# Performance work log

Measured on AMD Instinct MI355X. Metric: run time of the kernel, lower is better.

The kernel has to match this reference:

```python
import jax, jax.numpy as jnp
import numpy as np

D = 2048
N_HEADS = 16
N_KV = 4
HEAD_DIM = D // N_HEADS  # 128
N_REP = N_HEADS // N_KV  # 4
B, S = 2, 2048


def setup_inputs() -> dict:
    key = jax.random.key(0)
    ks = jax.random.split(key, 5)
    scale = 0.02
    return {
        "x": jax.random.normal(ks[0], (B, S, D), dtype=jnp.float32),
        "wq": jax.random.normal(ks[1], (D, N_HEADS * HEAD_DIM), dtype=jnp.float32) * scale,
        "wk": jax.random.normal(ks[2], (D, N_KV * HEAD_DIM), dtype=jnp.float32) * scale,
        "wv": jax.random.normal(ks[3], (D, N_KV * HEAD_DIM), dtype=jnp.float32) * scale,
        "wo": jax.random.normal(ks[4], (N_HEADS * HEAD_DIM, D), dtype=jnp.float32) * scale,
    }


def reference(x, wq, wk, wv, wo):
    b, s, _ = x.shape
    # projections
    xq = (x @ wq).reshape(b, s, N_HEADS, HEAD_DIM)
    xk = (x @ wk).reshape(b, s, N_KV, HEAD_DIM)
    xv = (x @ wv).reshape(b, s, N_KV, HEAD_DIM)
    # GQA: group queries per kv head -> [b, n_kv, n_rep, s, d]
    xq = xq.transpose(0, 2, 1, 3).reshape(b, N_KV, N_REP, s, HEAD_DIM)
    xk = xk.transpose(0, 2, 1, 3)  # [b, n_kv, s, d]
    xv = xv.transpose(0, 2, 1, 3)
    scale = 1.0 / jnp.sqrt(jnp.asarray(HEAD_DIM, dtype=x.dtype))
    scores = jnp.einsum('bkrqd,bkvd->bkrqv', xq, xk) * scale  # [b,n_kv,n_rep,s,s]
    causal = jnp.triu(jnp.ones((s, s), dtype=bool), k=1)
    scores = jnp.where(causal, jnp.asarray(-jnp.inf, dtype=scores.dtype), scores)
    probs = jax.nn.softmax(scores, axis=-1)
    out = jnp.einsum('bkrqv,bkvd->bkrqd', probs, xv)  # [b,n_kv,n_rep,s,d]
    out = out.reshape(b, N_HEADS, s, HEAD_DIM).transpose(0, 2, 1, 3).reshape(b, s, N_HEADS * HEAD_DIM)
    return out @ wo
```

## Files before the change

kernel.cpp:

```cpp
#include <hip/hip_runtime.h>

typedef unsigned short u16;
using bf16x8 = __attribute__((ext_vector_type(8))) short;
using bf16x4 = __attribute__((ext_vector_type(4))) short;
using f32x4  = __attribute__((ext_vector_type(4))) float;

#define ATTN_NEG (-3.0e38f)

#if __has_builtin(__builtin_amdgcn_mfma_f32_16x16x16_bf16)
__device__ __forceinline__ f32x4 mfma16(bf16x4 a, bf16x4 b, f32x4 c) {
  return __builtin_amdgcn_mfma_f32_16x16x16_bf16(a, b, c, 0, 0, 0);
}
#elif __has_builtin(__builtin_amdgcn_mfma_f32_16x16x16bf16_1k)
__device__ __forceinline__ f32x4 mfma16(bf16x4 a, bf16x4 b, f32x4 c) {
  return __builtin_amdgcn_mfma_f32_16x16x16bf16_1k(a, b, c, 0, 0, 0);
}
#else
__device__ __forceinline__ f32x4 mfma16(bf16x4 a, bf16x4 b, f32x4 c) {
  asm volatile("v_mfma_f32_16x16x16_bf16 %0, %1, %2, %3"
               : "=v"(c) : "v"(a), "v"(b), "v"(c));
  return c;
}
#endif

__device__ __forceinline__ u16 f2bf_rne(float f) {
  unsigned int u = __float_as_uint(f);
  u += 0x7fffu + ((u >> 16) & 1u);
  return (u16)(u >> 16);
}

__device__ __forceinline__ void load_lds16(const u16* g, u16* l) {
  using gp = const __attribute__((address_space(1))) unsigned int*;
  using lp = __attribute__((address_space(3))) unsigned int*;
  __builtin_amdgcn_global_load_lds((gp)g, (lp)l, 16, 0, 0);
}

__device__ __forceinline__ void transpose_body(const float* __restrict__ in,
                                               u16* __restrict__ out, int K, int N,
                                               int bx, int by, int tid) {
  __shared__ float tile[32][33];
  int tx = tid & 31, ty = tid >> 5;
  int x0 = bx * 32, y0 = by * 32;
  #pragma unroll
  for (int i = 0; i < 32; i += 8)
    tile[ty + i][tx] = in[(size_t)(y0 + ty + i) * N + x0 + tx];
  __syncthreads();
  #pragma unroll
  for (int i = 0; i < 32; i += 8)
    out[(size_t)(x0 + ty + i) * K + y0 + tx] = f2bf_rne(tile[tx][ty + i]);
}

__global__ __launch_bounds__(256) void prep_kernel(const float* __restrict__ x,
                                                   const float* __restrict__ wq,
                                                   const float* __restrict__ wk,
                                                   const float* __restrict__ wv,
                                                   const float* __restrict__ wo,
                                                   u16* xb, u16* wqt, u16* wkt, u16* wvt,
                                                   u16* wot) {
  int bid = blockIdx.x, tid = threadIdx.x;
  if (bid < 8192) {
    int i = bid * 1024 + tid * 4;
    float4 v = *(const float4*)(x + i);
    u16* p = xb + i;
    p[0] = f2bf_rne(v.x); p[1] = f2bf_rne(v.y); p[2] = f2bf_rne(v.z); p[3] = f2bf_rne(v.w);
  } else if (bid < 12288) {
    int t = bid - 8192;
    transpose_body(wq, wqt, 2048, 2048, t & 63, t >> 6, tid);
  } else if (bid < 13312) {
    int t = bid - 12288;
    transpose_body(wk, wkt, 2048, 512, t & 15, t >> 4, tid);
  } else if (bid < 14336) {
    int t = bid - 13312;
    transpose_body(wv, wvt, 2048, 512, t & 15, t >> 4, tid);
  } else {
    int t = bid - 14336;
    transpose_body(wo, wot, 2048, 2048, t & 63, t >> 6, tid);
  }
}

template <int MODE>
__device__ __forceinline__ void gemm_tile(const u16* __restrict__ A, const u16* __restrict__ Bt,
                                          void* __restrict__ Cv, int M, int N, int K,
                                          int bx, int by, char* smem) {
  u16* As = (u16*)smem;
  u16* Bs = (u16*)(smem + 8192);
  const int tid  = threadIdx.x;
  const int wave = tid >> 6, lane = tid & 63;
  const int quad = lane >> 4, l16 = lane & 15;
  const int m0 = by * 128, n0 = bx * 128;
  const int wm = (wave >> 1) * 64, wn = (wave & 1) * 64;
  f32x4 acc[4][4] = {};

  const int srow = (wave << 4) + (lane >> 2);
  const int scol = (lane & 3) << 3;
  const u16* ga0 = A  + (size_t)(m0 + srow) * K + scol;
  const u16* gb0 = Bt + (size_t)(n0 + srow) * K + scol;
  u16* la = As + wave * 512;
  u16* lb = Bs + wave * 512;

  for (int k0 = 0; k0 < K; k0 += 32) {
    __syncthreads();
    load_lds16(ga0 + k0, la);
    load_lds16(ga0 + (size_t)64 * K + k0, la + 2048);
    load_lds16(gb0 + k0, lb);
    load_lds16(gb0 + (size_t)64 * K + k0, lb + 2048);
    __syncthreads();
    bf16x8 af[4], bfr[4];
    #pragma unroll
    for (int i = 0; i < 4; ++i) {
      af[i]  = *(const bf16x8*)(As + (wm + i * 16 + l16) * 32 + quad * 8);
      bfr[i] = *(const bf16x8*)(Bs + (wn + i * 16 + l16) * 32 + quad * 8);
    }
    #pragma unroll
    for (int mi = 0; mi < 4; ++mi)
      #pragma unroll
      for (int ni = 0; ni < 4; ++ni)
        acc[mi][ni] = __builtin_amdgcn_mfma_f32_16x16x32_bf16(af[mi], bfr[ni], acc[mi][ni], 0, 0, 0);
  }

  if constexpr (MODE == 0 || MODE == 3) {
    const float sc = (MODE == 3) ? 0.12751742f : 1.0f;
    u16* Cb = (u16*)Cv;
    #pragma unroll
    for (int mi = 0; mi < 4; ++mi)
      #pragma unroll
      for (int ni = 0; ni < 4; ++ni) {
        int row = m0 + wm + mi * 16 + quad * 4;
        int col = n0 + wn + ni * 16 + l16;
        #pragma unroll
        for (int r = 0; r < 4; ++r)
          Cb[(size_t)(row + r) * N + col] = f2bf_rne(acc[mi][ni][r] * sc);
      }
  } else if constexpr (MODE == 1) {
    u16* Cb = (u16*)Cv;
    #pragma unroll
    for (int mi = 0; mi < 4; ++mi)
      #pragma unroll
      for (int ni = 0; ni < 4; ++ni) {
        int col = n0 + wn + ni * 16 + l16;
        #pragma unroll
        for (int r = 0; r < 4; ++r) {
          int row = m0 + wm + mi * 16 + quad * 4 + r;
          int bb = row >> 11, s = row & 2047;
          int c = s & 31;
          int cp = ((c & 15) >> 2) * 8 + ((c >> 4) & 1) * 4 + (c & 3);
          Cb[((size_t)(bb * 512 + col)) * 2048 + (s & ~31) + cp] = f2bf_rne(acc[mi][ni][r]);
        }
      }
  } else {
    float* Cf = (float*)Cv;
    #pragma unroll
    for (int mi = 0; mi < 4; ++mi)
      #pragma unroll
      for (int ni = 0; ni < 4; ++ni) {
        int row = m0 + wm + mi * 16 + quad * 4;
        int col = n0 + wn + ni * 16 + l16;
        #pragma unroll
        for (int r = 0; r < 4; ++r)
          Cf[(size_t)(row + r) * N + col] = acc[mi][ni][r];
      }
  }
}

__global__ __launch_bounds__(256) void qkv_gemm(const u16* xb, const u16* wqt, const u16* wkt,
                                                const u16* wvt, u16* Qb, u16* Kb, u16* Vt) {
  extern __shared__ char smem[];
  int bx = blockIdx.x, by = blockIdx.y;
  if (bx < 16)
    gemm_tile<3>(xb, wqt, Qb, 4096, 2048, 2048, bx, by, smem);
  else if (bx < 20)
    gemm_tile<0>(xb, wkt, Kb, 4096, 512, 2048, bx - 16, by, smem);
  else
    gemm_tile<1>(xb, wvt, Vt, 4096, 512, 2048, bx - 20, by, smem);
}

template <int MODE>
__global__ __launch_bounds__(256) void gemm_kernel(const u16* A, const u16* Bt, void* C,
                                                   int M, int N, int K) {
  extern __shared__ char smem[];
  gemm_tile<MODE>(A, Bt, C, M, N, K, blockIdx.x, blockIdx.y, smem);
}


__device__ __forceinline__ void stage_kv(const u16* __restrict__ Kg, const u16* __restrict__ Vg,
                                         int kt0, u16* __restrict__ kbuf, u16* __restrict__ vbuf,
                                         int wave, int quad, int l16) {
  #pragma unroll
  for (int h = 0; h < 2; ++h)
    load_lds16(Kg + (size_t)(kt0 + h * 16 + l16) * 512 + wave * 32 + quad * 8,
               kbuf + (wave * 2 + h) * 512);
  #pragma unroll
  for (int i = 0; i < 2; ++i) {
    int f = wave * 2 + i;
    load_lds16(Vg + (size_t)(16 * f + l16) * 2048 + kt0 + quad * 8, vbuf + f * 512);
  }
}

template <bool MASKED>
__device__ __forceinline__ void attn_compute(const u16* __restrict__ kbuf,
                                             const u16* __restrict__ vbuf,
                                             int kt0, int q0w, int quad, int l16,
                                             const bf16x8 (&qf)[4], f32x4 (&o)[8],
                                             float& l_lane) {
  const int slot = (quad * 16 + l16) * 8;
  bf16x8 kf[8];
  #pragma unroll
  for (int kk = 0; kk < 8; ++kk) kf[kk] = *(const bf16x8*)(kbuf + kk * 512 + slot);

  f32x4 sa[2] = {};
  #pragma unroll
  for (int h = 0; h < 2; ++h)
    #pragma unroll
    for (int ks = 0; ks < 4; ++ks)
      sa[h] = __builtin_amdgcn_mfma_f32_16x16x32_bf16(kf[ks * 2 + h], qf[ks], sa[h], 0, 0, 0);

  bf16x4 pa[2];
  #pragma unroll
  for (int h = 0; h < 2; ++h) {
    #pragma unroll
    for (int r = 0; r < 4; ++r) {
      float s = sa[h][r];
      if (MASKED) {
        int kpos = kt0 + 16 * h + quad * 4 + r;
        s = (kpos <= q0w + l16) ? s : ATTN_NEG;
      }
      float p = __builtin_amdgcn_exp2f(s);
      l_lane += p;
      pa[h][r] = (short)f2bf_rne(p);
    }
  }

  #pragma unroll
  for (int f = 0; f < 8; ++f) {
    bf16x8 v8 = *(const bf16x8*)(vbuf + f * 512 + slot);
    bf16x4 vlo = {v8[0], v8[1], v8[2], v8[3]};
    bf16x4 vhi = {v8[4], v8[5], v8[6], v8[7]};
    o[f] = mfma16(pa[0], vlo, o[f]);
    o[f] = mfma16(pa[1], vhi, o[f]);
  }
}

__global__ __launch_bounds__(256, 2) void attn_kernel(const u16* __restrict__ Qb,
                                                      const u16* __restrict__ Kb,
                                                      const u16* __restrict__ Vt,
                                                      u16* __restrict__ Ob) {
  constexpr int S = 2048;
  const int b = blockIdx.z, h = blockIdx.y, g = h >> 2, tp = blockIdx.x;
  const int tid = threadIdx.x;
  const int wave = tid >> 6, lane = tid & 63, quad = lane >> 4, l16 = lane & 15;
  __shared__ alignas(16) u16 Kt[2][4096];
  __shared__ alignas(16) u16 Vl[2][4096];
  __shared__ float lbuf[4][16];

  const u16* Kg = Kb + (size_t)b * S * 512 + g * 128;
  const u16* Vg = Vt + (size_t)(b * 512 + g * 128) * 2048;

  #pragma unroll
  for (int half = 0; half < 2; ++half) {
    const int tile = (half == 0) ? tp : 31 - tp;
    const int wrow = (half == 0) ? wave : 3 - wave;
    const int q0w = tile * 64 + wrow * 16;
    const int nsteps = 2 * tile + 2;
    const int s_diag = 2 * tile + (wrow >> 1);

    bf16x8 qf[4];
    const u16* qrow = Qb + (size_t)(b * S + q0w + l16) * 2048 + h * 128 + quad * 8;
    #pragma unroll
    for (int ks = 0; ks < 4; ++ks) qf[ks] = *(const bf16x8*)(qrow + ks * 32);

    f32x4 o[8] = {};
    float l_lane = 0.f;

    __syncthreads();
    stage_kv(Kg, Vg, 0, Kt[0], Vl[0], wave, quad, l16);

    for (int s = 0; s < nsteps; ++s) {
      __syncthreads();
      if (s + 1 < nsteps)
        stage_kv(Kg, Vg, (s + 1) * 32, Kt[(s + 1) & 1], Vl[(s + 1) & 1], wave, quad, l16);
      if (s < s_diag)
        attn_compute<false>(Kt[s & 1], Vl[s & 1], s * 32, q0w, quad, l16, qf, o, l_lane);
      else if (s == s_diag)
        attn_compute<true>(Kt[s & 1], Vl[s & 1], s * 32, q0w, quad, l16, qf, o, l_lane);
    }

    float lt = l_lane + __shfl_xor(l_lane, 16);
    lt += __shfl_xor(lt, 32);
    if (quad == 0) lbuf[wave][l16] = lt;
    __builtin_amdgcn_wave_barrier();
    float il[4];
    #pragma unroll
    for (int r = 0; r < 4; ++r) il[r] = 1.f / lbuf[wave][quad * 4 + r];

    u16* orow = Ob + (size_t)(b * S + q0w + quad * 4) * 2048 + h * 128 + l16;
    #pragma unroll
    for (int f = 0; f < 8; ++f)
      #pragma unroll
      for (int r = 0; r < 4; ++r)
        orow[(size_t)r * 2048 + f * 16] = f2bf_rne(o[f][r] * il[r]);
  }
}

extern "C" void kernel_launch(void* const* d_in, const int* in_sizes, int n_in,
                              void* d_out, int out_size, void* d_ws, size_t ws_size,
                              hipStream_t stream) {
  const float* x  = (const float*)d_in[0];
  const float* wq = (const float*)d_in[1];
  const float* wk = (const float*)d_in[2];
  const float* wv = (const float*)d_in[3];
  const float* wo = (const float*)d_in[4];
  float* out = (float*)d_out;
  char* ws = (char*)d_ws;

  u16* xb  = (u16*)(ws);
  u16* wqt = (u16*)(ws + 16777216);
  u16* wkt = (u16*)(ws + 25165824);
  u16* wvt = (u16*)(ws + 27262976);
  u16* wot = (u16*)(ws + 29360128);
  u16* Qb  = (u16*)(ws + 37748736);
  u16* Kb  = (u16*)(ws + 54525952);
  u16* Vt  = (u16*)(ws + 58720256);
  u16* Ab  = (u16*)(ws + 62914560);

  prep_kernel<<<18432, 256, 0, stream>>>(x, wq, wk, wv, wo, xb, wqt, wkt, wvt, wot);
  qkv_gemm<<<dim3(24, 32), 256, 16384, stream>>>(xb, wqt, wkt, wvt, Qb, Kb, Vt);
  attn_kernel<<<dim3(16, 16, 2), 256, 0, stream>>>(Qb, Kb, Vt, Ab);
  gemm_kernel<2><<<dim3(16, 32), 256, 16384, stream>>>(Ab, wot, out, 4096, 2048, 2048);
}
```

Baseline: 311.8 us.

## Split KV steps across wave pairs with 32-row query tiles and LDS merge

Result: slower. 331.9 us (+6.5%).

```diff
diff --git a/kernel.cpp b/kernel.cpp
--- a/kernel.cpp
+++ b/kernel.cpp
@@ -197,46 +197,54 @@
 }
 
 template <bool MASKED>
-__device__ __forceinline__ void attn_compute(const u16* __restrict__ kbuf,
-                                             const u16* __restrict__ vbuf,
-                                             int kt0, int q0w, int quad, int l16,
-                                             const bf16x8 (&qf)[4], f32x4 (&o)[8],
-                                             float& l_lane) {
+__device__ __forceinline__ void attn_compute2(const u16* __restrict__ kbuf,
+                                              const u16* __restrict__ vbuf,
+                                              int kt0, int q0p, int quad, int l16,
+                                              const bf16x8 (&qf)[2][4], f32x4 (&o)[2][8],
+                                              float (&l_lane)[2]) {
   const int slot = (quad * 16 + l16) * 8;
   bf16x8 kf[8];
   #pragma unroll
   for (int kk = 0; kk < 8; ++kk) kf[kk] = *(const bf16x8*)(kbuf + kk * 512 + slot);
 
-  f32x4 sa[2] = {};
-  #pragma unroll
-  for (int h = 0; h < 2; ++h)
-    #pragma unroll
-    for (int ks = 0; ks < 4; ++ks)
-      sa[h] = __builtin_amdgcn_mfma_f32_16x16x32_bf16(kf[ks * 2 + h], qf[ks], sa[h], 0, 0, 0);
-
-  bf16x4 pa[2];
-  #pragma unroll
-  for (int h = 0; h < 2; ++h) {
-    #pragma unroll
-    for (int r = 0; r < 4; ++r) {
-      float s = sa[h][r];
-      if (MASKED) {
-        int kpos = kt0 + 16 * h + quad * 4 + r;
-        s = (kpos <= q0w + l16) ? s : ATTN_NEG;
-      }
-      float p = __builtin_amdgcn_exp2f(s);
-      l_lane += p;
-      pa[h][r] = (short)f2bf_rne(p);
-    }
-  }
+  f32x4 sa[2][2] = {};
+  #pragma unroll
+  for (int j = 0; j < 2; ++j)
+    #pragma unroll
+    for (int h = 0; h < 2; ++h)
+      #pragma unroll
+      for (int ks = 0; ks < 4; ++ks)
+        sa[j][h] = __builtin_amdgcn_mfma_f32_16x16x32_bf16(kf[ks * 2 + h], qf[j][ks],
+                                                           sa[j][h], 0, 0, 0);
+
+  bf16x4 pa[2][2];
+  #pragma unroll
+  for (int j = 0; j < 2; ++j)
+    #pragma unroll
+    for (int h = 0; h < 2; ++h) {
+      #pragma unroll
+      for (int r = 0; r < 4; ++r) {
+        float s = sa[j][h][r];
+        if (MASKED) {
+          int kpos = kt0 + 16 * h + quad * 4 + r;
+          s = (kpos <= q0p + j * 16 + l16) ? s : ATTN_NEG;
+        }
+        float p = __builtin_amdgcn_exp2f(s);
+        l_lane[j] += p;
+        pa[j][h][r] = (short)f2bf_rne(p);
+      }
+    }
 
   #pragma unroll
   for (int f = 0; f < 8; ++f) {
     bf16x8 v8 = *(const bf16x8*)(vbuf + f * 512 + slot);
     bf16x4 vlo = {v8[0], v8[1], v8[2], v8[3]};
     bf16x4 vhi = {v8[4], v8[5], v8[6], v8[7]};
-    o[f] = mfma16(pa[0], vlo, o[f]);
-    o[f] = mfma16(pa[1], vhi, o[f]);
+    #pragma unroll
+    for (int j = 0; j < 2; ++j) {
+      o[j][f] = mfma16(pa[j][0], vlo, o[j][f]);
+      o[j][f] = mfma16(pa[j][1], vhi, o[j][f]);
+    }
   }
 }
 
@@ -248,56 +256,94 @@
   const int b = blockIdx.z, h = blockIdx.y, g = h >> 2, tp = blockIdx.x;
   const int tid = threadIdx.x;
   const int wave = tid >> 6, lane = tid & 63, quad = lane >> 4, l16 = lane & 15;
-  __shared__ alignas(16) u16 Kt[2][4096];
-  __shared__ alignas(16) u16 Vl[2][4096];
-  __shared__ float lbuf[4][16];
+  const int pair = wave >> 1, wpar = wave & 1;
+  __shared__ alignas(16) u16 sraw[16384];
+  __shared__ float lmrg[2][128];
+  __shared__ float lbuf[2][2][16];
+
+  u16* Ktb = sraw;
+  u16* Vlb = sraw + 8192;
 
   const u16* Kg = Kb + (size_t)b * S * 512 + g * 128;
   const u16* Vg = Vt + (size_t)(b * 512 + g * 128) * 2048;
 
-  #pragma unroll
   for (int half = 0; half < 2; ++half) {
     const int tile = (half == 0) ? tp : 31 - tp;
-    const int wrow = (half == 0) ? wave : 3 - wave;
-    const int q0w = tile * 64 + wrow * 16;
+    const int q0p = tile * 64 + pair * 32;
     const int nsteps = 2 * tile + 2;
-    const int s_diag = 2 * tile + (wrow >> 1);
-
-    bf16x8 qf[4];
-    const u16* qrow = Qb + (size_t)(b * S + q0w + l16) * 2048 + h * 128 + quad * 8;
-    #pragma unroll
-    for (int ks = 0; ks < 4; ++ks) qf[ks] = *(const bf16x8*)(qrow + ks * 32);
-
-    f32x4 o[8] = {};
-    float l_lane = 0.f;
-
-    __syncthreads();
-    stage_kv(Kg, Vg, 0, Kt[0], Vl[0], wave, quad, l16);
+    const int s_diag = 2 * tile + pair;
+    const int par = wpar ^ half;
+
+    bf16x8 qf[2][4];
+    #pragma unroll
+    for (int j = 0; j < 2; ++j) {
+      const u16* qrow = Qb + (size_t)(b * S + q0p + j * 16 + l16) * 2048 + h * 128 + quad * 8;
+      #pragma unroll
+      for (int ks = 0; ks < 4; ++ks) qf[j][ks] = *(const bf16x8*)(qrow + ks * 32);
+    }
+
+    f32x4 o[2][8] = {};
+    float l_lane[2] = {0.f, 0.f};
+
+    __syncthreads();
+    stage_kv(Kg, Vg, 0, Ktb, Vlb, wave, quad, l16);
 
     for (int s = 0; s < nsteps; ++s) {
       __syncthreads();
+      const u16* kb = Ktb + (s & 1) * 4096;
+      const u16* vb = Vlb + (s & 1) * 4096;
       if (s + 1 < nsteps)
-        stage_kv(Kg, Vg, (s + 1) * 32, Kt[(s + 1) & 1], Vl[(s + 1) & 1], wave, quad, l16);
-      if (s < s_diag)
-        attn_compute<false>(Kt[s & 1], Vl[s & 1], s * 32, q0w, quad, l16, qf, o, l_lane);
-      else if (s == s_diag)
-        attn_compute<true>(Kt[s & 1], Vl[s & 1], s * 32, q0w, quad, l16, qf, o, l_lane);
-    }
-
-    float lt = l_lane + __shfl_xor(l_lane, 16);
-    lt += __shfl_xor(lt, 32);
-    if (quad == 0) lbuf[wave][l16] = lt;
-    __builtin_amdgcn_wave_barrier();
-    float il[4];
-    #pragma unroll
-    for (int r = 0; r < 4; ++r) il[r] = 1.f / lbuf[wave][quad * 4 + r];
-
-    u16* orow = Ob + (size_t)(b * S + q0w + quad * 4) * 2048 + h * 128 + l16;
-    #pragma unroll
-    for (int f = 0; f < 8; ++f)
-      #pragma unroll
-      for (int r = 0; r < 4; ++r)
-        orow[(size_t)r * 2048 + f * 16] = f2bf_rne(o[f][r] * il[r]);
+        stage_kv(Kg, Vg, (s + 1) * 32, Ktb + ((s + 1) & 1) * 4096,
+                 Vlb + ((s + 1) & 1) * 4096, wave, quad, l16);
+      if (((s & 1) == par) && s <= s_diag) {
+        if (s == s_diag)
+          attn_compute2<true>(kb, vb, s * 32, q0p, quad, l16, qf, o, l_lane);
+        else
+          attn_compute2<false>(kb, vb, s * 32, q0p, quad, l16, qf, o, l_lane);
+      }
+    }
+
+    __syncthreads();
+    if (wpar) {
+      float* mb = (float*)sraw + pair * 4096 + lane * 64;
+      #pragma unroll
+      for (int j = 0; j < 2; ++j)
+        #pragma unroll
+        for (int f = 0; f < 8; ++f)
+          *(f32x4*)(mb + j * 32 + f * 4) = o[j][f];
+      lmrg[pair][lane] = l_lane[0];
+      lmrg[pair][64 + lane] = l_lane[1];
+    }
+    __syncthreads();
+    if (!wpar) {
+      const float* mb = (const float*)sraw + pair * 4096 + lane * 64;
+      #pragma unroll
+      for (int j = 0; j < 2; ++j) {
+        #pragma unroll
+        for (int f = 0; f < 8; ++f) {
+          f32x4 t = *(const f32x4*)(mb + j * 32 + f * 4);
+          #pragma unroll
+          for (int r = 0; r < 4; ++r) o[j][f][r] += t[r];
+        }
+        float lt = l_lane[j] + lmrg[pair][j * 64 + lane];
+        lt += __shfl_xor(lt, 16);
+        lt += __shfl_xor(lt, 32);
+        if (quad == 0) lbuf[pair][j][l16] = lt;
+      }
+      __builtin_amdgcn_wave_barrier();
+      #pragma unroll
+      for (int j = 0; j < 2; ++j) {
+        float il[4];
+        #pragma unroll
+        for (int r = 0; r < 4; ++r) il[r] = 1.f / lbuf[pair][j][quad * 4 + r];
+        u16* orow = Ob + (size_t)(b * S + q0p + j * 16 + quad * 4) * 2048 + h * 128 + l16;
+        #pragma unroll
+        for (int f = 0; f < 8; ++f)
+          #pragma unroll
+          for (int r = 0; r < 4; ++r)
+            orow[(size_t)r * 2048 + f * 16] = f2bf_rne(o[j][f][r] * il[r]);
+      }
+    }
   }
 }
 
```
